# Performance work log

Measured on AMD Instinct MI355X. Metric: run time of the kernel, lower is better.

The kernel has to match this reference:

```python
import jax, jax.numpy as jnp
import numpy as np

TEMPERATURE = 2.0


def _offdiag_idx(n):
    # flat indices of the off-diagonal entries of an [n, n] matrix, row-major,
    # reshaped to [n, n-1] (matches torch masked_select(~eye).view(n, n-1))
    idx = np.arange(n * n).reshape(n, n)
    return jnp.asarray(idx[~np.eye(n, dtype=bool)].reshape(n, n - 1))


def setup_inputs() -> dict:
    key = jax.random.key(0)
    k1, k2, k3, k4 = jax.random.split(key, 4)
    B, D = 256, 512
    return {
        "wt_emb": jax.random.normal(k1, (B, D), dtype=jnp.float32),
        "mt_emb": jax.random.normal(k2, (B, D), dtype=jnp.float32),
        "label_wt": jax.random.uniform(k3, (B,), dtype=jnp.float32),
        "label_mt": jax.random.uniform(k4, (B,), dtype=jnp.float32),
    }


def reference(wt_emb, mt_emb, label_wt, label_mt):
    t = TEMPERATURE
    features = jnp.concatenate([wt_emb, mt_emb], axis=0)            # [n, D]
    labels = jnp.concatenate([label_wt, label_mt], axis=0)[:, None]  # [n, 1]
    n = features.shape[0]

    # L1 label differences: [n, n]
    label_diffs = jnp.abs(labels[:, None, :] - labels[None, :, :]).sum(-1)

    # negative L2 feature distances (safe sqrt: diagonal is exactly 0)
    diff = features[:, None, :] - features[None, :, :]               # [n, n, D]
    sq = jnp.sum(diff * diff, axis=-1)                               # [n, n]
    dist = jnp.where(sq > 0, jnp.sqrt(jnp.where(sq > 0, sq, 1.0)), 0.0)
    logits = -dist / t
    logits = logits - jax.lax.stop_gradient(jnp.max(logits, axis=1, keepdims=True))
    exp_logits = jnp.exp(logits)

    # drop diagonal -> [n, n-1]
    off = _offdiag_idx(n)
    lo = logits.reshape(-1)[off]
    eo = exp_logits.reshape(-1)[off]
    ldo = label_diffs.reshape(-1)[off]

    # vectorized over positive index k: mask[i, k, j] = ld[i, j] >= ld[i, k]
    neg_mask = ldo[:, None, :] >= ldo[:, :, None]                    # [n, n-1, n-1]
    denom = jnp.sum(jnp.where(neg_mask, eo[:, None, :], 0.0), axis=-1)  # [n, n-1]
    pos_log_probs = lo - jnp.log(denom)                              # [n, n-1]
    return -jnp.sum(pos_log_probs) / (n * (n - 1))
```

## Files before the change

kernel.cpp:

```cpp
#include <hip/hip_runtime.h>

#define N 512
#define B 256
#define D 512
#define NT 512
#define NBLK (N / 2)

#define WS_SL    0
#define WS_NORM  512
#define WS_PART  1024
#define WS_FS    2048

__global__ __launch_bounds__(NT) void sort_rows_kernel(
    const float* __restrict__ wt, const float* __restrict__ mt,
    const float* __restrict__ lwt, const float* __restrict__ lmt,
    float* __restrict__ ws)
{
    const int t = threadIdx.x, b = blockIdx.x;
    __shared__ float slab[N];
    __shared__ int scnt[32];
    slab[t] = (t < B) ? lwt[t] : lmt[t - B];
    if (t < 32) scnt[t] = 0;
    __syncthreads();

    const int jj = t & 31, j = b * 32 + jj, c = t >> 5;
    const float lj = slab[j];
    int r = 0;
    #pragma unroll 8
    for (int x = c * 32; x < c * 32 + 32; ++x) {
        const float v = slab[x];
        r += (v < lj || (v == lj && x < j)) ? 1 : 0;
    }
    atomicAdd(&scnt[jj], r);
    __syncthreads();

    if (t < 32)
        ws[WS_SL + scnt[t]] = slab[b * 32 + t];

    const int row = b * 32 + (t >> 4), s16 = t & 15;
    const int rr = scnt[t >> 4];
    const float* F = (row < B) ? (wt + (size_t)row * D) : (mt + (size_t)(row - B) * D);
    const float4* F4 = (const float4*)F;
    float4* Dst = (float4*)(ws + WS_FS + (size_t)rr * D);
    float nacc = 0.f;
    #pragma unroll
    for (int q = 0; q < 8; ++q) {
        const int idx = s16 + 16 * q;
        const float4 v = F4[idx];
        nacc += v.x * v.x + v.y * v.y + v.z * v.z + v.w * v.w;
        Dst[idx] = v;
    }
    nacc += __shfl_down(nacc, 8, 16);
    nacc += __shfl_down(nacc, 4, 16);
    nacc += __shfl_down(nacc, 2, 16);
    nacc += __shfl_down(nacc, 1, 16);
    if (s16 == 0) ws[WS_NORM + rr] = nacc;
}

__global__ __launch_bounds__(NT) void rnc_main(
    float* __restrict__ ws)
{
    const int b = blockIdx.x, i0 = 2 * b, i1 = 2 * b + 1;
    const int t = threadIdx.x;
    const int w = t >> 6, lane = t & 63, g = lane >> 4, s = lane & 15;

    __shared__ float sl[N];
    __shared__ float snm[N];
    __shared__ __align__(16) float sp0[N];
    __shared__ __align__(16) float sf0[N];
    __shared__ __align__(16) float sp1[N];
    __shared__ __align__(16) float sf1[N];
    __shared__ float sred[NT / 64];

    sl[t]  = ws[WS_SL + t];
    snm[t] = ws[WS_NORM + t];

    const float* Fs = ws + WS_FS;
    const float4* Fi04 = (const float4*)(Fs + (size_t)i0 * D);
    const float4* Fi14 = (const float4*)(Fs + (size_t)i1 * D);
    float4 fr0[8], fr1[8];
    #pragma unroll
    for (int q = 0; q < 8; ++q) { fr0[q] = Fi04[s + 16 * q]; fr1[q] = Fi14[s + 16 * q]; }
    __syncthreads();
    const float li0 = sl[i0], li1 = sl[i1];
    const float ni0 = snm[i0], ni1 = snm[i1];

    float lg_acc = 0.f;
    const int wg = w * 4 + g;
    for (int m = 0; m < 16; ++m) {
        const int j = wg + 32 * m;
        const float4* Fj4 = (const float4*)(Fs + (size_t)j * D);
        float a0 = 0.f, a1 = 0.f;
        #pragma unroll
        for (int q = 0; q < 8; ++q) {
            const float4 v = Fj4[s + 16 * q];
            a0 += fr0[q].x * v.x + fr0[q].y * v.y + fr0[q].z * v.z + fr0[q].w * v.w;
            a1 += fr1[q].x * v.x + fr1[q].y * v.y + fr1[q].z * v.z + fr1[q].w * v.w;
        }
        a0 += __shfl_down(a0, 8, 16); a1 += __shfl_down(a1, 8, 16);
        a0 += __shfl_down(a0, 4, 16); a1 += __shfl_down(a1, 4, 16);
        a0 += __shfl_down(a0, 2, 16); a1 += __shfl_down(a1, 2, 16);
        a0 += __shfl_down(a0, 1, 16); a1 += __shfl_down(a1, 1, 16);
        if (s == 0) {
            const float nj = snm[j];
            const float d0 = fmaxf(ni0 + nj - 2.f * a0, 0.f);
            const float d1 = fmaxf(ni1 + nj - 2.f * a1, 0.f);
            const float lg0 = -0.5f * sqrtf(d0);
            const float lg1 = -0.5f * sqrtf(d1);
            if (j != i0) lg_acc += lg0;
            if (j != i1) lg_acc += lg1;
            const float e0 = (j == i0) ? 0.f : __expf(lg0);
            const float e1 = (j == i1) ? 0.f : __expf(lg1);
            sp0[j] = e0; sf0[j] = e0;
            sp1[j] = e1; sf1[j] = e1;
        }
    }
    __syncthreads();

    if (w < 4) {
        float* arr = (w == 0) ? sp0 : (w == 1) ? sf0 : (w == 2) ? sp1 : sf1;
        float4* a4 = (float4*)arr;
        float4 u0 = a4[lane * 2], u1 = a4[lane * 2 + 1];
        float v0 = u0.x, v1 = u0.y, v2 = u0.z, v3 = u0.w;
        float v4 = u1.x, v5 = u1.y, v6 = u1.z, v7 = u1.w;
        if ((w & 1) == 0) {
            v1 += v0; v2 += v1; v3 += v2; v4 += v3; v5 += v4; v6 += v5; v7 += v6;
            float x = v7;
            #pragma unroll
            for (int off = 1; off < 64; off <<= 1) {
                const float y = __shfl_up(x, off, 64);
                if (lane >= off) x += y;
            }
            float ex = __shfl_up(x, 1, 64);
            if (lane == 0) ex = 0.f;
            v0 += ex; v1 += ex; v2 += ex; v3 += ex; v4 += ex; v5 += ex; v6 += ex; v7 += ex;
        } else {
            v6 += v7; v5 += v6; v4 += v5; v3 += v4; v2 += v3; v1 += v2; v0 += v1;
            float x = v0;
            #pragma unroll
            for (int off = 1; off < 64; off <<= 1) {
                const float y = __shfl_down(x, off, 64);
                if (lane + off < 64) x += y;
            }
            float ex = __shfl_down(x, 1, 64);
            if (lane == 63) ex = 0.f;
            v0 += ex; v1 += ex; v2 += ex; v3 += ex; v4 += ex; v5 += ex; v6 += ex; v7 += ex;
        }
        a4[lane * 2]     = make_float4(v0, v1, v2, v3);
        a4[lane * 2 + 1] = make_float4(v4, v5, v6, v7);
    }
    __syncthreads();

    float local = lg_acc;
    #pragma unroll
    for (int p = 0; p < 2; ++p) {
        const int idx = t + p * NT;
        const int row = idx >> 9;
        const int x = idx & (N - 1);
        const int ri = row ? i1 : i0;
        const float li = row ? li1 : li0;
        const float* SP = row ? sp1 : sp0;
        const float* SF = row ? sf1 : sf0;
        if (x != ri) {
            const float th = fabsf(li - sl[x]);
            int lo = 0, hi = ri + 1;
            while (lo < hi) {
                const int mid = (lo + hi) >> 1;
                if (fabsf(li - sl[mid]) >= th) lo = mid + 1; else hi = mid;
            }
            const int a = lo;
            lo = ri + 1; hi = N;
            while (lo < hi) {
                const int mid = (lo + hi) >> 1;
                if (fabsf(li - sl[mid]) >= th) hi = mid; else lo = mid + 1;
            }
            const int bb = lo;
            const float denom = ((a > 0) ? SP[a - 1] : 0.f) + ((bb < N) ? SF[bb] : 0.f);
            local -= __logf(denom);
        }
    }

    #pragma unroll
    for (int off = 32; off > 0; off >>= 1)
        local += __shfl_down(local, off, 64);
    if (lane == 0) sred[w] = local;
    __syncthreads();
    if (t == 0) {
        float sum = 0.f;
        #pragma unroll
        for (int k = 0; k < NT / 64; ++k) sum += sred[k];
        ws[WS_PART + b] = sum;
    }
}

__global__ __launch_bounds__(NBLK) void rnc_finalize(
    const float* __restrict__ ws, float* __restrict__ out)
{
    const int t = threadIdx.x;
    __shared__ float sred[NBLK / 64];
    float v = ws[WS_PART + t];
    #pragma unroll
    for (int off = 32; off > 0; off >>= 1)
        v += __shfl_down(v, off, 64);
    if ((t & 63) == 0) sred[t >> 6] = v;
    __syncthreads();
    if (t == 0) {
        float sum = 0.f;
        #pragma unroll
        for (int k = 0; k < NBLK / 64; ++k) sum += sred[k];
        out[0] = -sum / (float)((long)N * (N - 1));
    }
}

extern "C" void kernel_launch(void* const* d_in, const int* in_sizes, int n_in,
                              void* d_out, int out_size, void* d_ws, size_t ws_size,
                              hipStream_t stream) {
    const float* wt  = (const float*)d_in[0];
    const float* mt  = (const float*)d_in[1];
    const float* lwt = (const float*)d_in[2];
    const float* lmt = (const float*)d_in[3];
    float* out = (float*)d_out;
    float* ws  = (float*)d_ws;

    sort_rows_kernel<<<16, NT, 0, stream>>>(wt, mt, lwt, lmt, ws);
    rnc_main<<<NBLK, NT, 0, stream>>>(ws);
    rnc_finalize<<<1, NBLK, 0, stream>>>(ws, out);
}
```

Baseline: 83.22 us.

## Compute Gram matrix with fp16 MFMA in a separate kernel

Features are stored as fp16 in the sort kernel, and a new kernel computes the full 512x512 Gram matrix with 16x16x32 f16 MFMA instructions, writing it to workspace. The main kernel then reads one Gram entry per thread instead of doing per-block fp32 dot products over all rows. This removes redundant feature reads and scalar FMAs across blocks, at the cost of an extra launch, a 1 MB Gram round-trip through memory, and fp16 precision loss in the distances.

```diff
diff --git a/kernel.cpp b/kernel.cpp
--- a/kernel.cpp
+++ b/kernel.cpp
@@ -9,7 +9,12 @@
 #define WS_SL    0
 #define WS_NORM  512
 #define WS_PART  1024
-#define WS_FS    2048
+#define WS_FH    2048
+#define WS_G     (2048 + (N * D) / 2)
+
+typedef _Float16 half4_t  __attribute__((ext_vector_type(4)));
+typedef _Float16 half8_t  __attribute__((ext_vector_type(8)));
+typedef float    f32x4    __attribute__((ext_vector_type(4)));
 
 __global__ __launch_bounds__(NT) void sort_rows_kernel(
     const float* __restrict__ wt, const float* __restrict__ mt,
@@ -41,14 +46,19 @@
     const int rr = scnt[t >> 4];
     const float* F = (row < B) ? (wt + (size_t)row * D) : (mt + (size_t)(row - B) * D);
     const float4* F4 = (const float4*)F;
-    float4* Dst = (float4*)(ws + WS_FS + (size_t)rr * D);
+    half4_t* Dst = (half4_t*)((_Float16*)(ws + WS_FH) + (size_t)rr * D);
     float nacc = 0.f;
     #pragma unroll
     for (int q = 0; q < 8; ++q) {
         const int idx = s16 + 16 * q;
         const float4 v = F4[idx];
-        nacc += v.x * v.x + v.y * v.y + v.z * v.z + v.w * v.w;
-        Dst[idx] = v;
+        half4_t h;
+        h[0] = (_Float16)v.x; h[1] = (_Float16)v.y;
+        h[2] = (_Float16)v.z; h[3] = (_Float16)v.w;
+        const float f0 = (float)h[0], f1 = (float)h[1];
+        const float f2 = (float)h[2], f3 = (float)h[3];
+        nacc += f0 * f0 + f1 * f1 + f2 * f2 + f3 * f3;
+        Dst[idx] = h;
     }
     nacc += __shfl_down(nacc, 8, 16);
     nacc += __shfl_down(nacc, 4, 16);
@@ -57,12 +67,36 @@
     if (s16 == 0) ws[WS_NORM + rr] = nacc;
 }
 
-__global__ __launch_bounds__(NT) void rnc_main(
-    float* __restrict__ ws)
+__global__ __launch_bounds__(256) void gram_kernel(float* __restrict__ ws)
+{
+    const int lane = threadIdx.x & 63;
+    const int wid  = blockIdx.x * 4 + (threadIdx.x >> 6);
+    const int ti = wid >> 5, tj = wid & 31;
+    const int quad = lane >> 4, m = lane & 15;
+
+    const _Float16* Fh = (const _Float16*)(ws + WS_FH);
+    const _Float16* Arow = Fh + (size_t)(ti * 16 + m) * D + quad * 8;
+    const _Float16* Brow = Fh + (size_t)(tj * 16 + m) * D + quad * 8;
+
+    f32x4 acc = {0.f, 0.f, 0.f, 0.f};
+    #pragma unroll
+    for (int k0 = 0; k0 < D; k0 += 32) {
+        const half8_t a = *(const half8_t*)(Arow + k0);
+        const half8_t b = *(const half8_t*)(Brow + k0);
+        acc = __builtin_amdgcn_mfma_f32_16x16x32_f16(a, b, acc, 0, 0, 0);
+    }
+    float* G = ws + WS_G;
+    const int col = tj * 16 + m;
+    #pragma unroll
+    for (int rg = 0; rg < 4; ++rg)
+        G[(size_t)(ti * 16 + quad * 4 + rg) * N + col] = acc[rg];
+}
+
+__global__ __launch_bounds__(NT) void rnc_main(float* __restrict__ ws)
 {
     const int b = blockIdx.x, i0 = 2 * b, i1 = 2 * b + 1;
     const int t = threadIdx.x;
-    const int w = t >> 6, lane = t & 63, g = lane >> 4, s = lane & 15;
+    const int w = t >> 6, lane = t & 63;
 
     __shared__ float sl[N];
     __shared__ float snm[N];
@@ -74,47 +108,24 @@
 
     sl[t]  = ws[WS_SL + t];
     snm[t] = ws[WS_NORM + t];
-
-    const float* Fs = ws + WS_FS;
-    const float4* Fi04 = (const float4*)(Fs + (size_t)i0 * D);
-    const float4* Fi14 = (const float4*)(Fs + (size_t)i1 * D);
-    float4 fr0[8], fr1[8];
-    #pragma unroll
-    for (int q = 0; q < 8; ++q) { fr0[q] = Fi04[s + 16 * q]; fr1[q] = Fi14[s + 16 * q]; }
     __syncthreads();
     const float li0 = sl[i0], li1 = sl[i1];
     const float ni0 = snm[i0], ni1 = snm[i1];
 
+    const float* G = ws + WS_G;
+    const float g0 = G[(size_t)i0 * N + t];
+    const float g1 = G[(size_t)i1 * N + t];
+    const float d0 = fmaxf(ni0 + snm[t] - 2.f * g0, 0.f);
+    const float d1 = fmaxf(ni1 + snm[t] - 2.f * g1, 0.f);
+    const float lg0 = -0.5f * sqrtf(d0);
+    const float lg1 = -0.5f * sqrtf(d1);
     float lg_acc = 0.f;
-    const int wg = w * 4 + g;
-    for (int m = 0; m < 16; ++m) {
-        const int j = wg + 32 * m;
-        const float4* Fj4 = (const float4*)(Fs + (size_t)j * D);
-        float a0 = 0.f, a1 = 0.f;
-        #pragma unroll
-        for (int q = 0; q < 8; ++q) {
-            const float4 v = Fj4[s + 16 * q];
-            a0 += fr0[q].x * v.x + fr0[q].y * v.y + fr0[q].z * v.z + fr0[q].w * v.w;
-            a1 += fr1[q].x * v.x + fr1[q].y * v.y + fr1[q].z * v.z + fr1[q].w * v.w;
-        }
-        a0 += __shfl_down(a0, 8, 16); a1 += __shfl_down(a1, 8, 16);
-        a0 += __shfl_down(a0, 4, 16); a1 += __shfl_down(a1, 4, 16);
-        a0 += __shfl_down(a0, 2, 16); a1 += __shfl_down(a1, 2, 16);
-        a0 += __shfl_down(a0, 1, 16); a1 += __shfl_down(a1, 1, 16);
-        if (s == 0) {
-            const float nj = snm[j];
-            const float d0 = fmaxf(ni0 + nj - 2.f * a0, 0.f);
-            const float d1 = fmaxf(ni1 + nj - 2.f * a1, 0.f);
-            const float lg0 = -0.5f * sqrtf(d0);
-            const float lg1 = -0.5f * sqrtf(d1);
-            if (j != i0) lg_acc += lg0;
-            if (j != i1) lg_acc += lg1;
-            const float e0 = (j == i0) ? 0.f : __expf(lg0);
-            const float e1 = (j == i1) ? 0.f : __expf(lg1);
-            sp0[j] = e0; sf0[j] = e0;
-            sp1[j] = e1; sf1[j] = e1;
-        }
-    }
+    if (t != i0) lg_acc += lg0;
+    if (t != i1) lg_acc += lg1;
+    const float e0 = (t == i0) ? 0.f : __expf(lg0);
+    const float e1 = (t == i1) ? 0.f : __expf(lg1);
+    sp0[t] = e0; sf0[t] = e0;
+    sp1[t] = e1; sf1[t] = e1;
     __syncthreads();
 
     if (w < 4) {
@@ -154,13 +165,11 @@
     float local = lg_acc;
     #pragma unroll
     for (int p = 0; p < 2; ++p) {
-        const int idx = t + p * NT;
-        const int row = idx >> 9;
-        const int x = idx & (N - 1);
-        const int ri = row ? i1 : i0;
-        const float li = row ? li1 : li0;
-        const float* SP = row ? sp1 : sp0;
-        const float* SF = row ? sf1 : sf0;
+        const int x = t;
+        const int ri = p ? i1 : i0;
+        const float li = p ? li1 : li0;
+        const float* SP = p ? sp1 : sp0;
+        const float* SF = p ? sf1 : sf0;
         if (x != ri) {
             const float th = fabsf(li - sl[x]);
             int lo = 0, hi = ri + 1;
@@ -223,6 +232,7 @@
     float* ws  = (float*)d_ws;
 
     sort_rows_kernel<<<16, NT, 0, stream>>>(wt, mt, lwt, lmt, ws);
+    gram_kernel<<<256, 256, 0, stream>>>(ws);
     rnc_main<<<NBLK, NT, 0, stream>>>(ws);
     rnc_finalize<<<1, NBLK, 0, stream>>>(ws, out);
 }
```

Measured after the change: 74.84 us. -10.1%, faster.
